# Performance work log

Hardware: AMD Instinct MI355X
Metric: run time of the kernel (lower is better)

Reference implementation:

```python
import jax, jax.numpy as jnp
import numpy as np

K_TOP = 2  # module's top-k


def setup_inputs() -> dict:
    key = jax.random.key(0)
    ks = jax.random.split(key, 6)
    s = 0.02
    B, S, H, D = 4, 1024, 2048, 1024
    E_SH, E_RT = 2, 16
    return {
        "x": jax.random.normal(ks[0], (B, S, H), dtype=jnp.float32),
        "Wsh_up": jax.random.normal(ks[1], (E_SH, H, D), dtype=jnp.float32) * s,
        "Wsh_down": jax.random.normal(ks[2], (E_SH, D, H), dtype=jnp.float32) * s,
        "Wrt_up": jax.random.normal(ks[3], (E_RT, H, D), dtype=jnp.float32) * s,
        "Wrt_down": jax.random.normal(ks[4], (E_RT, D, H), dtype=jnp.float32) * s,
        "W_router": jax.random.normal(ks[5], (H, E_RT), dtype=jnp.float32) * s,
    }


def reference(x, Wsh_up, Wsh_down, Wrt_up, Wrt_down, W_router):
    B, S, H = x.shape
    E_rt = Wrt_up.shape[0]
    xt = x.reshape(B * S, H)  # [T,H]

    # shared experts (summed)
    sh_mid = jax.nn.gelu(jnp.einsum('th,ehd->ted', xt, Wsh_up), approximate=False)
    shared_out = jnp.einsum('ted,edh->th', sh_mid, Wsh_down)  # [T,H]

    # router: softmax over all routed experts, then top-k
    probs = jax.nn.softmax(xt @ W_router, axis=-1)  # [T,E]
    top_v, top_i = jax.lax.top_k(probs, K_TOP)  # [T,K]
    # per-token dense gate weights over experts (zero for non-selected)
    gate = jnp.sum(jax.nn.one_hot(top_i, E_rt, dtype=xt.dtype) * top_v[..., None], axis=1)  # [T,E]

    # routed experts: compute all experts densely, combine with sparse gate
    rt_mid = jax.nn.gelu(jnp.einsum('th,ehd->ted', xt, Wrt_up), approximate=False)  # [T,E,D]
    routed_out = jnp.einsum('ted,edh->th', rt_mid * gate[:, :, None], Wrt_down)  # [T,H]

    return (shared_out + routed_out).reshape(B, S, H)
```

## Files before the change

### kernel.cpp

```cpp
#include <hip/hip_runtime.h>
#include <cstdint>
#include <cstddef>

typedef __bf16 bf16_t;
typedef __bf16 bf16x8 __attribute__((ext_vector_type(8)));
typedef float floatx4 __attribute__((ext_vector_type(4)));

static constexpr int T_TOK = 4096;
static constexpr int HDIM  = 2048;
static constexpr int DDIM  = 1024;
static constexpr int ESH   = 2;
static constexpr int ERT   = 16;
static constexpr int NPAIR = 2 * T_TOK;
static constexpr int NPAIR_PAD = NPAIR + 128;

__device__ __forceinline__ float gelu_f(float v) {
  return 0.5f * v * (1.0f + erff(v * 0.70710678118654752440f));
}

__global__ __launch_bounds__(256) void router_kernel(
    const float* __restrict__ x, const float* __restrict__ Wr,
    int* __restrict__ top_e, float* __restrict__ top_w, int* __restrict__ counts)
{
  const int t = blockIdx.x;
  const int tid = threadIdx.x;
  float acc[ERT];
#pragma unroll
  for (int e = 0; e < ERT; ++e) acc[e] = 0.f;
  const float* xr = x + (long)t * HDIM;
  for (int h = tid; h < HDIM; h += 256) {
    const float xv = xr[h];
    const float4* w4 = (const float4*)(Wr + h * ERT);
    const float4 w0 = w4[0], w1 = w4[1], w2 = w4[2], w3 = w4[3];
    acc[0]  += xv * w0.x; acc[1]  += xv * w0.y; acc[2]  += xv * w0.z; acc[3]  += xv * w0.w;
    acc[4]  += xv * w1.x; acc[5]  += xv * w1.y; acc[6]  += xv * w1.z; acc[7]  += xv * w1.w;
    acc[8]  += xv * w2.x; acc[9]  += xv * w2.y; acc[10] += xv * w2.z; acc[11] += xv * w2.w;
    acc[12] += xv * w3.x; acc[13] += xv * w3.y; acc[14] += xv * w3.z; acc[15] += xv * w3.w;
  }
  __shared__ float s[256][ERT + 1];
#pragma unroll
  for (int e = 0; e < ERT; ++e) s[tid][e] = acc[e];
  __syncthreads();
  for (int st = 128; st >= 1; st >>= 1) {
    if (tid < st) {
#pragma unroll
      for (int e = 0; e < ERT; ++e) s[tid][e] += s[tid + st][e];
    }
    __syncthreads();
  }
  if (tid == 0) {
    float l[ERT];
    float mx = -1e30f;
#pragma unroll
    for (int e = 0; e < ERT; ++e) { l[e] = s[0][e]; mx = fmaxf(mx, l[e]); }
    float sum = 0.f;
#pragma unroll
    for (int e = 0; e < ERT; ++e) { l[e] = expf(l[e] - mx); sum += l[e]; }
    const float inv = 1.f / sum;
    float v0 = -1.f, v1 = -1.f; int i0 = 0, i1 = 0;
#pragma unroll
    for (int e = 0; e < ERT; ++e) {
      const float p = l[e] * inv;
      if (p > v0) { v1 = v0; i1 = i0; v0 = p; i0 = e; }
      else if (p > v1) { v1 = p; i1 = e; }
    }
    top_e[2 * t] = i0; top_e[2 * t + 1] = i1;
    top_w[2 * t] = v0; top_w[2 * t + 1] = v1;
    atomicAdd(&counts[i0], 1); atomicAdd(&counts[i1], 1);
  }
}

__global__ void prefix_kernel(const int* __restrict__ counts, int* __restrict__ offsets) {
  if (threadIdx.x == 0) {
    int s = 0;
    for (int e = 0; e < ERT; ++e) { offsets[e] = s; s += counts[e]; }
    offsets[ERT] = s;
  }
}

__global__ __launch_bounds__(256) void scatter_kernel(
    const int* __restrict__ top_e, const float* __restrict__ top_w,
    const int* __restrict__ offsets, int* __restrict__ cursor,
    int* __restrict__ pair_token, float* __restrict__ pair_w,
    int* __restrict__ inv_slot)
{
  const int t = blockIdx.x * 256 + threadIdx.x;
  if (t >= T_TOK) return;
#pragma unroll
  for (int k = 0; k < 2; ++k) {
    const int e = top_e[2 * t + k];
    const int pos = atomicAdd(&cursor[e], 1);
    const int slot = offsets[e] + pos;
    pair_token[slot] = t;
    pair_w[slot] = top_w[2 * t + k];
    inv_slot[2 * t + k] = slot;
  }
}

__global__ __launch_bounds__(256) void cast_x_kernel(const float* __restrict__ x, bf16_t* __restrict__ xb) {
  const long base = (long)blockIdx.x * HDIM + threadIdx.x * 8;
  const float4 a = *(const float4*)(x + base);
  const float4 b = *(const float4*)(x + base + 4);
  bf16x8 v;
  v[0] = (__bf16)a.x; v[1] = (__bf16)a.y; v[2] = (__bf16)a.z; v[3] = (__bf16)a.w;
  v[4] = (__bf16)b.x; v[5] = (__bf16)b.y; v[6] = (__bf16)b.z; v[7] = (__bf16)b.w;
  *(bf16x8*)(xb + base) = v;
}

__global__ __launch_bounds__(256) void gather_kernel(
    const float* __restrict__ x, const int* __restrict__ pair_token, bf16_t* __restrict__ xg)
{
  const int slot = blockIdx.x;
  const int tok = pair_token[slot];
  const float* src = x + (long)tok * HDIM;
  const int c = threadIdx.x * 8;
  const float4 a = *(const float4*)(src + c);
  const float4 b = *(const float4*)(src + c + 4);
  bf16x8 v;
  v[0] = (__bf16)a.x; v[1] = (__bf16)a.y; v[2] = (__bf16)a.z; v[3] = (__bf16)a.w;
  v[4] = (__bf16)b.x; v[5] = (__bf16)b.y; v[6] = (__bf16)b.z; v[7] = (__bf16)b.w;
  *(bf16x8*)(xg + (long)slot * HDIM + c) = v;
}

__global__ __launch_bounds__(256) void transpose_cast_kernel(
    const float* __restrict__ in, bf16_t* __restrict__ out, int R, int C)
{
  __shared__ float tl[64][65];
  const long mat = blockIdx.z;
  in  += mat * (long)R * C;
  out += mat * (long)R * C;
  const int c0 = blockIdx.x * 64, r0 = blockIdx.y * 64;
  const int tid = threadIdx.x;
  const int lr = tid >> 4;
  const int lc4 = (tid & 15) * 4;
#pragma unroll
  for (int i = 0; i < 4; ++i) {
    const int r = lr + i * 16;
    const float4 v = *(const float4*)(in + (long)(r0 + r) * C + c0 + lc4);
    tl[r][lc4 + 0] = v.x; tl[r][lc4 + 1] = v.y; tl[r][lc4 + 2] = v.z; tl[r][lc4 + 3] = v.w;
  }
  __syncthreads();
#pragma unroll
  for (int i = 0; i < 4; ++i) {
    const int c = lr + i * 16;
    ushort4 o;
    o.x = __builtin_bit_cast(unsigned short, (__bf16)tl[lc4 + 0][c]);
    o.y = __builtin_bit_cast(unsigned short, (__bf16)tl[lc4 + 1][c]);
    o.z = __builtin_bit_cast(unsigned short, (__bf16)tl[lc4 + 2][c]);
    o.w = __builtin_bit_cast(unsigned short, (__bf16)tl[lc4 + 3][c]);
    *(ushort4*)((unsigned short*)out + (long)(c0 + c) * R + r0 + lc4) = o;
  }
}

__global__ __launch_bounds__(256) void combine_kernel(
    const bf16_t* __restrict__ sh_out, const bf16_t* __restrict__ pair_out,
    const int* __restrict__ inv_slot, float* __restrict__ out)
{
  const int t = blockIdx.x;
  const int c = threadIdx.x * 8;
  const int s0 = inv_slot[2 * t], s1 = inv_slot[2 * t + 1];
  const bf16x8 a = *(const bf16x8*)(sh_out  + (long)t  * HDIM + c);
  const bf16x8 b = *(const bf16x8*)(pair_out + (long)s0 * HDIM + c);
  const bf16x8 d = *(const bf16x8*)(pair_out + (long)s1 * HDIM + c);
  float4 o0, o1;
  o0.x = (float)a[0] + (float)b[0] + (float)d[0];
  o0.y = (float)a[1] + (float)b[1] + (float)d[1];
  o0.z = (float)a[2] + (float)b[2] + (float)d[2];
  o0.w = (float)a[3] + (float)b[3] + (float)d[3];
  o1.x = (float)a[4] + (float)b[4] + (float)d[4];
  o1.y = (float)a[5] + (float)b[5] + (float)d[5];
  o1.z = (float)a[6] + (float)b[6] + (float)d[6];
  o1.w = (float)a[7] + (float)b[7] + (float)d[7];
  *(float4*)(out + (long)t * HDIM + c) = o0;
  *(float4*)(out + (long)t * HDIM + c + 4) = o1;
}

template<int MODE>
__global__ __launch_bounds__(256) void gemm_kernel(
    const bf16_t* __restrict__ Abase, const bf16_t* __restrict__ Bbase,
    bf16_t* __restrict__ Cbf,
    const int* __restrict__ counts, const int* __restrict__ offsets,
    const float* __restrict__ pair_w)
{
  constexpr int K   = (MODE == 3) ? 1024 : 2048;
  constexpr int LDA = (MODE == 3) ? 1024 : 2048;
  constexpr int LDB = (MODE == 1 || MODE == 3) ? 1024 : 2048;

  const int mt = blockIdx.x, nt = blockIdx.y, e = blockIdx.z;
  const int m0 = mt * 128;
  int cnt = 0, segoff = 0;
  if (MODE == 2 || MODE == 3) {
    cnt = counts[e];
    if (m0 >= cnt) return;
    segoff = offsets[e];
  }

  const bf16_t* Ab;
  const bf16_t* Bb;
  if (MODE == 0) {
    Ab = Abase + (long)m0 * LDA;
    Bb = Bbase + (long)(nt >> 3) * ((long)DDIM * HDIM) + (long)((nt & 7) * 128) * LDB;
  } else if (MODE == 1) {
    Ab = Abase + (long)m0 * LDA;
    Bb = Bbase + (long)(nt * 128) * LDB;
  } else if (MODE == 2) {
    Ab = Abase + (long)(segoff + m0) * LDA;
    Bb = Bbase + (long)e * ((long)DDIM * HDIM) + (long)(nt * 128) * LDB;
  } else {
    Ab = Abase + (long)(segoff + m0) * LDA;
    Bb = Bbase + (long)e * ((long)HDIM * DDIM) + (long)(nt * 128) * LDB;
  }

  __shared__ bf16_t As[128 * 72];
  __shared__ bf16_t Bs[128 * 72];

  const int tid = threadIdx.x;
  const int rr = tid >> 3, ch = tid & 7;
  const int lane = tid & 63, wv = tid >> 6;
  const int ln = lane & 15, quad = lane >> 4;
  const int wm = (wv & 1) * 64, wn = (wv >> 1) * 64;

  floatx4 acc[4][4];
#pragma unroll
  for (int i = 0; i < 4; ++i)
#pragma unroll
    for (int j = 0; j < 4; ++j) acc[i][j] = (floatx4){0.f, 0.f, 0.f, 0.f};

  for (int k0 = 0; k0 < K; k0 += 64) {
    bf16x8 av[4], bv[4];
    long bkoff;
    if (MODE == 1) bkoff = (long)(k0 >> 10) * ((long)HDIM * DDIM) + (k0 & 1023);
    else bkoff = k0;
#pragma unroll
    for (int i = 0; i < 4; ++i) {
      av[i] = *(const bf16x8*)(Ab + (long)(rr + i * 32) * LDA + k0 + ch * 8);
      bv[i] = *(const bf16x8*)(Bb + (long)(rr + i * 32) * LDB + bkoff + ch * 8);
    }
    __syncthreads();
#pragma unroll
    for (int i = 0; i < 4; ++i) {
      *(bf16x8*)(&As[(rr + i * 32) * 72 + ch * 8]) = av[i];
      *(bf16x8*)(&Bs[(rr + i * 32) * 72 + ch * 8]) = bv[i];
    }
    __syncthreads();
#pragma unroll
    for (int s = 0; s < 2; ++s) {
      bf16x8 af[4], bfr[4];
      const int ko = s * 32 + quad * 8;
#pragma unroll
      for (int mf = 0; mf < 4; ++mf) af[mf]  = *(const bf16x8*)(&As[(wm + mf * 16 + ln) * 72 + ko]);
#pragma unroll
      for (int nf = 0; nf < 4; ++nf) bfr[nf] = *(const bf16x8*)(&Bs[(wn + nf * 16 + ln) * 72 + ko]);
#pragma unroll
      for (int mf = 0; mf < 4; ++mf)
#pragma unroll
        for (int nf = 0; nf < 4; ++nf)
          acc[mf][nf] = __builtin_amdgcn_mfma_f32_16x16x32_bf16(af[mf], bfr[nf], acc[mf][nf], 0, 0, 0);
    }
  }

#pragma unroll
  for (int mf = 0; mf < 4; ++mf) {
#pragma unroll
    for (int r = 0; r < 4; ++r) {
      const int rl = wm + mf * 16 + quad * 4 + r;
      const int gm = m0 + rl;
      if ((MODE == 2 || MODE == 3) && gm >= cnt) continue;
      float wgt = 0.f;
      if (MODE == 2) wgt = pair_w[segoff + gm];
#pragma unroll
      for (int nf = 0; nf < 4; ++nf) {
        const int clg = nt * 128 + wn + nf * 16 + ln;
        const float v = acc[mf][nf][r];
        if (MODE == 0)      Cbf[(long)gm * 2048 + clg] = (__bf16)gelu_f(v);
        else if (MODE == 1) Cbf[(long)gm * 2048 + clg] = (__bf16)v;
        else if (MODE == 2) Cbf[(long)(segoff + gm) * 1024 + clg] = (__bf16)(gelu_f(v) * wgt);
        else                Cbf[(long)(segoff + gm) * 2048 + clg] = (__bf16)v;
      }
    }
  }
}

extern "C" void kernel_launch(void* const* d_in, const int* in_sizes, int n_in,
                              void* d_out, int out_size, void* d_ws, size_t ws_size,
                              hipStream_t stream)
{
  (void)in_sizes; (void)n_in; (void)out_size; (void)ws_size;
  const float* x        = (const float*)d_in[0];
  const float* Wsh_up   = (const float*)d_in[1];
  const float* Wsh_down = (const float*)d_in[2];
  const float* Wrt_up   = (const float*)d_in[3];
  const float* Wrt_down = (const float*)d_in[4];
  const float* Wr       = (const float*)d_in[5];
  float* out = (float*)d_out;

  char* w = (char*)d_ws;
  size_t off = 0;
  auto alloc = [&](size_t bytes) -> void* {
    void* p = w + off;
    off = (off + bytes + 255) & ~(size_t)255;
    return p;
  };
  int*    counts  = (int*)alloc(64);
  int*    cursor  = (int*)alloc(64);
  int*    offsets = (int*)alloc(128);
  int*    top_e   = (int*)alloc((size_t)2 * T_TOK * 4);
  float*  top_w   = (float*)alloc((size_t)2 * T_TOK * 4);
  int*    pair_token = (int*)alloc((size_t)NPAIR_PAD * 4);
  float*  pair_w  = (float*)alloc((size_t)NPAIR_PAD * 4);
  int*    inv_slot = (int*)alloc((size_t)2 * T_TOK * 4);
  bf16_t* xb      = (bf16_t*)alloc((size_t)T_TOK * HDIM * 2);
  bf16_t* xg      = (bf16_t*)alloc((size_t)NPAIR_PAD * HDIM * 2);
  bf16_t* midsh   = (bf16_t*)alloc((size_t)T_TOK * (ESH * DDIM) * 2);
  bf16_t* midrt   = (bf16_t*)alloc((size_t)NPAIR_PAD * DDIM * 2);
  bf16_t* WshUt   = (bf16_t*)alloc((size_t)ESH * DDIM * HDIM * 2);
  bf16_t* WshDt   = (bf16_t*)alloc((size_t)ESH * HDIM * DDIM * 2);
  bf16_t* WrtUt   = (bf16_t*)alloc((size_t)ERT * DDIM * HDIM * 2);
  bf16_t* WrtDt   = (bf16_t*)alloc((size_t)ERT * HDIM * DDIM * 2);
  bf16_t* sh_out   = xb;
  bf16_t* pair_out = xg;

  hipMemsetAsync(w, 0, 768, stream);

  router_kernel<<<T_TOK, 256, 0, stream>>>(x, Wr, top_e, top_w, counts);
  prefix_kernel<<<1, 64, 0, stream>>>(counts, offsets);
  scatter_kernel<<<T_TOK / 256, 256, 0, stream>>>(top_e, top_w, offsets, cursor,
                                                  pair_token, pair_w, inv_slot);
  cast_x_kernel<<<T_TOK, 256, 0, stream>>>(x, xb);
  gather_kernel<<<NPAIR, 256, 0, stream>>>(x, pair_token, xg);

  transpose_cast_kernel<<<dim3(DDIM / 64, HDIM / 64, ESH), 256, 0, stream>>>(Wsh_up,   WshUt, HDIM, DDIM);
  transpose_cast_kernel<<<dim3(HDIM / 64, DDIM / 64, ESH), 256, 0, stream>>>(Wsh_down, WshDt, DDIM, HDIM);
  transpose_cast_kernel<<<dim3(DDIM / 64, HDIM / 64, ERT), 256, 0, stream>>>(Wrt_up,   WrtUt, HDIM, DDIM);
  transpose_cast_kernel<<<dim3(HDIM / 64, DDIM / 64, ERT), 256, 0, stream>>>(Wrt_down, WrtDt, DDIM, HDIM);

  gemm_kernel<0><<<dim3(32, 16, 1), 256, 0, stream>>>(xb, WshUt, midsh,
                                                      nullptr, nullptr, nullptr);
  gemm_kernel<2><<<dim3(32, 8, ERT), 256, 0, stream>>>(xg, WrtUt, midrt,
                                                       counts, offsets, pair_w);
  gemm_kernel<1><<<dim3(32, 16, 1), 256, 0, stream>>>(midsh, WshDt, sh_out,
                                                      nullptr, nullptr, nullptr);
  gemm_kernel<3><<<dim3(32, 16, ERT), 256, 0, stream>>>(midrt, WrtDt, pair_out,
                                                        counts, offsets, nullptr);
  combine_kernel<<<T_TOK, 256, 0, stream>>>(sh_out, pair_out, inv_slot, out);
}
```

Baseline: 1.241 ms.

## Merge shared and routed expert GEMMs into one launch per phase with register prefetch

```diff
diff --git a/kernel.cpp b/kernel.cpp
--- a/kernel.cpp
+++ b/kernel.cpp
@@ -175,40 +175,48 @@
   *(float4*)(out + (long)t * HDIM + c + 4) = o1;
 }
 
-template<int MODE>
-__global__ __launch_bounds__(256) void gemm_kernel(
-    const bf16_t* __restrict__ Abase, const bf16_t* __restrict__ Bbase,
-    bf16_t* __restrict__ Cbf,
+template<int PHASE>
+__global__ __launch_bounds__(256) void gemm_fused(
+    const bf16_t* __restrict__ Ash, const bf16_t* __restrict__ Art,
+    const bf16_t* __restrict__ Bsh, const bf16_t* __restrict__ Brt,
+    bf16_t* __restrict__ Csh, bf16_t* __restrict__ Crt,
     const int* __restrict__ counts, const int* __restrict__ offsets,
     const float* __restrict__ pair_w)
 {
-  constexpr int K   = (MODE == 3) ? 1024 : 2048;
-  constexpr int LDA = (MODE == 3) ? 1024 : 2048;
-  constexpr int LDB = (MODE == 1 || MODE == 3) ? 1024 : 2048;
-
-  const int mt = blockIdx.x, nt = blockIdx.y, e = blockIdx.z;
+  const int mt = blockIdx.x, nt = blockIdx.y;
+  const bool is_sh = (blockIdx.z == 0);
+  const int e = (int)blockIdx.z - 1;
   const int m0 = mt * 128;
-  int cnt = 0, segoff = 0;
-  if (MODE == 2 || MODE == 3) {
-    cnt = counts[e];
-    if (m0 >= cnt) return;
-    segoff = offsets[e];
-  }
-
-  const bf16_t* Ab;
-  const bf16_t* Bb;
-  if (MODE == 0) {
-    Ab = Abase + (long)m0 * LDA;
-    Bb = Bbase + (long)(nt >> 3) * ((long)DDIM * HDIM) + (long)((nt & 7) * 128) * LDB;
-  } else if (MODE == 1) {
-    Ab = Abase + (long)m0 * LDA;
-    Bb = Bbase + (long)(nt * 128) * LDB;
-  } else if (MODE == 2) {
-    Ab = Abase + (long)(segoff + m0) * LDA;
-    Bb = Bbase + (long)e * ((long)DDIM * HDIM) + (long)(nt * 128) * LDB;
+
+  int K, lda, ldb, cnt = 0, segoff = 0;
+  const bf16_t *Ab, *Bb;
+  if (PHASE == 0) {
+    if (is_sh) {
+      K = 2048; lda = 2048; ldb = 2048;
+      Ab = Ash + (long)m0 * 2048;
+      Bb = Bsh + (long)nt * 128 * 2048;
+    } else {
+      if (nt >= 8) return;
+      cnt = counts[e];
+      if (m0 >= cnt) return;
+      segoff = offsets[e];
+      K = 2048; lda = 2048; ldb = 2048;
+      Ab = Art + (long)(segoff + m0) * 2048;
+      Bb = Brt + (long)e * (1024L * 2048) + (long)nt * 128 * 2048;
+    }
   } else {
-    Ab = Abase + (long)(segoff + m0) * LDA;
-    Bb = Bbase + (long)e * ((long)HDIM * DDIM) + (long)(nt * 128) * LDB;
+    if (is_sh) {
+      K = 2048; lda = 2048; ldb = 1024;
+      Ab = Ash + (long)m0 * 2048;
+      Bb = Bsh + (long)nt * 128 * 1024;
+    } else {
+      cnt = counts[e];
+      if (m0 >= cnt) return;
+      segoff = offsets[e];
+      K = 1024; lda = 1024; ldb = 1024;
+      Ab = Art + (long)(segoff + m0) * 1024;
+      Bb = Brt + (long)e * (2048L * 1024) + (long)nt * 128 * 1024;
+    }
   }
 
   __shared__ bf16_t As[128 * 72];
@@ -226,16 +234,17 @@
 #pragma unroll
     for (int j = 0; j < 4; ++j) acc[i][j] = (floatx4){0.f, 0.f, 0.f, 0.f};
 
+  bf16x8 av[4], bv[4];
+  {
+    long bk = (PHASE == 1 && is_sh) ? 0L : 0L;
+#pragma unroll
+    for (int i = 0; i < 4; ++i) {
+      av[i] = *(const bf16x8*)(Ab + (long)(rr + i * 32) * lda + ch * 8);
+      bv[i] = *(const bf16x8*)(Bb + (long)(rr + i * 32) * ldb + bk + ch * 8);
+    }
+  }
+
   for (int k0 = 0; k0 < K; k0 += 64) {
-    bf16x8 av[4], bv[4];
-    long bkoff;
-    if (MODE == 1) bkoff = (long)(k0 >> 10) * ((long)HDIM * DDIM) + (k0 & 1023);
-    else bkoff = k0;
-#pragma unroll
-    for (int i = 0; i < 4; ++i) {
-      av[i] = *(const bf16x8*)(Ab + (long)(rr + i * 32) * LDA + k0 + ch * 8);
-      bv[i] = *(const bf16x8*)(Bb + (long)(rr + i * 32) * LDB + bkoff + ch * 8);
-    }
     __syncthreads();
 #pragma unroll
     for (int i = 0; i < 4; ++i) {
@@ -243,6 +252,19 @@
       *(bf16x8*)(&Bs[(rr + i * 32) * 72 + ch * 8]) = bv[i];
     }
     __syncthreads();
+
+    const int kn = k0 + 64;
+    if (kn < K) {
+      long bk;
+      if (PHASE == 1 && is_sh) bk = (long)(kn >> 10) * (2048L * 1024) + (kn & 1023);
+      else bk = kn;
+#pragma unroll
+      for (int i = 0; i < 4; ++i) {
+        av[i] = *(const bf16x8*)(Ab + (long)(rr + i * 32) * lda + kn + ch * 8);
+        bv[i] = *(const bf16x8*)(Bb + (long)(rr + i * 32) * ldb + bk + ch * 8);
+      }
+    }
+
 #pragma unroll
     for (int s = 0; s < 2; ++s) {
       bf16x8 af[4], bfr[4];
@@ -265,17 +287,20 @@
     for (int r = 0; r < 4; ++r) {
       const int rl = wm + mf * 16 + quad * 4 + r;
       const int gm = m0 + rl;
-      if ((MODE == 2 || MODE == 3) && gm >= cnt) continue;
+      if (!is_sh && gm >= cnt) continue;
       float wgt = 0.f;
-      if (MODE == 2) wgt = pair_w[segoff + gm];
+      if (PHASE == 0 && !is_sh) wgt = pair_w[segoff + gm];
 #pragma unroll
       for (int nf = 0; nf < 4; ++nf) {
         const int clg = nt * 128 + wn + nf * 16 + ln;
         const float v = acc[mf][nf][r];
-        if (MODE == 0)      Cbf[(long)gm * 2048 + clg] = (__bf16)gelu_f(v);
-        else if (MODE == 1) Cbf[(long)gm * 2048 + clg] = (__bf16)v;
-        else if (MODE == 2) Cbf[(long)(segoff + gm) * 1024 + clg] = (__bf16)(gelu_f(v) * wgt);
-        else                Cbf[(long)(segoff + gm) * 2048 + clg] = (__bf16)v;
+        if (PHASE == 0) {
+          if (is_sh) Csh[(long)gm * 2048 + clg] = (__bf16)gelu_f(v);
+          else       Crt[(long)(segoff + gm) * 1024 + clg] = (__bf16)(gelu_f(v) * wgt);
+        } else {
+          if (is_sh) Csh[(long)gm * 2048 + clg] = (__bf16)v;
+          else       Crt[(long)(segoff + gm) * 2048 + clg] = (__bf16)v;
+        }
       }
     }
   }
@@ -334,13 +359,10 @@
   transpose_cast_kernel<<<dim3(DDIM / 64, HDIM / 64, ERT), 256, 0, stream>>>(Wrt_up,   WrtUt, HDIM, DDIM);
   transpose_cast_kernel<<<dim3(HDIM / 64, DDIM / 64, ERT), 256, 0, stream>>>(Wrt_down, WrtDt, DDIM, HDIM);
 
-  gemm_kernel<0><<<dim3(32, 16, 1), 256, 0, stream>>>(xb, WshUt, midsh,
-                                                      nullptr, nullptr, nullptr);
-  gemm_kernel<2><<<dim3(32, 8, ERT), 256, 0, stream>>>(xg, WrtUt, midrt,
-                                                       counts, offsets, pair_w);
-  gemm_kernel<1><<<dim3(32, 16, 1), 256, 0, stream>>>(midsh, WshDt, sh_out,
-                                                      nullptr, nullptr, nullptr);
-  gemm_kernel<3><<<dim3(32, 16, ERT), 256, 0, stream>>>(midrt, WrtDt, pair_out,
-                                                        counts, offsets, nullptr);
+  gemm_fused<0><<<dim3(32, 16, 17), 256, 0, stream>>>(xb, xg, WshUt, WrtUt,
+                                                      midsh, midrt, counts, offsets, pair_w);
+  gemm_fused<1><<<dim3(32, 16, 17), 256, 0, stream>>>(midsh, midrt, WshDt, WrtDt,
+                                                      sh_out, pair_out, counts, offsets, nullptr);
+
   combine_kernel<<<T_TOK, 256, 0, stream>>>(sh_out, pair_out, inv_slot, out);
 }
```

Measured after the change: 1.281 ms. +3.2%, slower.
